# Kernel optimization log

Measured on AMD Instinct MI355X. Metric: run time of the kernel, lower is better.

## Reference

```python
import jax, jax.numpy as jnp
import numpy as np

N_FRAMES = 64
N_ATOMS = 512
SEG_LEN = 1


def get_segments(n_atoms: int, length: int) -> np.ndarray:
    """All ordered pairs of chain segments (i,i+L),(j,j+L) that share no atoms (j-i>L)."""
    starts = np.arange(n_atoms - length)
    i, j = np.meshgrid(starts, starts, indexing='ij')
    mask = (j - i) > length
    i, j = i[mask], j[mask]
    return np.stack([i, i + length, j, j + length], axis=1).astype(np.int32)


def setup_inputs() -> dict:
    key = jax.random.key(0)
    xyz = jax.random.normal(key, (N_FRAMES, N_ATOMS, 3), dtype=jnp.float32)
    segments = jnp.asarray(get_segments(N_ATOMS, SEG_LEN))  # (P, 4) int32
    return {"xyz": xyz, "segments": segments}


def _unit(v):
    return v / jnp.linalg.norm(v, axis=-1, keepdims=True)


def reference(xyz, segments):
    # xyz: (F, N, 3); segments: (P, 4) = [i, i+L, j, j+L]
    p1 = xyz[:, segments[:, 0]]  # (F, P, 3)
    p2 = xyz[:, segments[:, 1]]
    p3 = xyz[:, segments[:, 2]]
    p4 = xyz[:, segments[:, 3]]

    r12 = p2 - p1
    r13 = p3 - p1
    r14 = p4 - p1
    r23 = p3 - p2
    r24 = p4 - p2
    r34 = p4 - p3

    # unit normals of the four faces of the tetrahedron spanned by the segment pair
    n1 = _unit(jnp.cross(r13, r14))
    n2 = _unit(jnp.cross(r14, r24))
    n3 = _unit(jnp.cross(r24, r23))
    n4 = _unit(jnp.cross(r23, r13))

    def asin_dot(a, b):
        return jnp.arcsin(jnp.clip(jnp.sum(a * b, axis=-1), -1.0, 1.0))

    # Gauss linking integral (Klenin & Langowski) per segment pair
    theta = asin_dot(n1, n2) + asin_dot(n2, n3) + asin_dot(n3, n4) + asin_dot(n4, n1)
    sign = jnp.sign(jnp.sum(jnp.cross(r34, r12) * r13, axis=-1))
    wr = theta * sign / (2.0 * jnp.pi)  # (F, P)
    return wr
```

## Files before the change

### kernel.cpp

```cpp
#include <hip/hip_runtime.h>
#include <math.h>

#define NFRAMES 64
#define NATOMS  512
#define NSEG    129795
#define NROWS   509
#define BLOCK   128
#define LDS_SLOTS 576

typedef float v2 __attribute__((ext_vector_type(2)));

__device__ __forceinline__ v2 v2s(float x) { v2 r; r.x = x; r.y = x; return r; }
__device__ __forceinline__ v2 vfma(v2 a, v2 b, v2 c) { return __builtin_elementwise_fma(a, b, c); }
__device__ __forceinline__ v2 vabs(v2 x) { v2 r; r.x = fabsf(x.x); r.y = fabsf(x.y); return r; }
__device__ __forceinline__ v2 vmin1(v2 a) { v2 r; r.x = fminf(a.x, 1.0f); r.y = fminf(a.y, 1.0f); return r; }
__device__ __forceinline__ v2 vsqrt_raw(v2 x) {
    v2 r; r.x = __builtin_amdgcn_sqrtf(x.x); r.y = __builtin_amdgcn_sqrtf(x.y); return r;
}
__device__ __forceinline__ v2 vrsq_raw(v2 x) {
    v2 r; r.x = __builtin_amdgcn_rsqf(x.x); r.y = __builtin_amdgcn_rsqf(x.y); return r;
}
__device__ __forceinline__ v2 vcopysign(v2 m, v2 s) {
    v2 r; r.x = copysignf(m.x, s.x); r.y = copysignf(m.y, s.y); return r;
}

__device__ __forceinline__ v2 vasin(v2 x) {
    v2 ax = vmin1(vabs(x));
    v2 p  = vfma(ax, vfma(ax, vfma(ax, v2s(-0.0187293f), v2s(0.0742610f)), v2s(-0.2121144f)), v2s(1.5707288f));
    v2 r  = v2s(1.57079632679f) - vsqrt_raw(v2s(1.0f) - ax) * p;
    return vcopysign(r, x);
}

struct v23 { v2 x, y, z; };

__device__ __forceinline__ v23 vsub(v23 a, v23 b) { return v23{a.x - b.x, a.y - b.y, a.z - b.z}; }
__device__ __forceinline__ v23 vcross(v23 a, v23 b) {
    return v23{ vfma(a.y, b.z, -(a.z * b.y)),
                vfma(a.z, b.x, -(a.x * b.z)),
                vfma(a.x, b.y, -(a.y * b.x)) };
}
__device__ __forceinline__ v2 vdot(v23 a, v23 b) {
    return vfma(a.x, b.x, vfma(a.y, b.y, a.z * b.z));
}

__device__ __forceinline__ v2 writhe2(const v23& p1, const v23& p2, const v23& p3, const v23& p4) {
    v23 r12 = vsub(p2, p1);
    v23 r13 = vsub(p3, p1);
    v23 r14 = vsub(p4, p1);
    v23 r23 = vsub(p3, p2);
    v23 r24 = vsub(p4, p2);
    v23 r34 = vsub(p4, p3);

    v23 c1 = vcross(r13, r14);
    v23 c2 = vcross(r14, r24);
    v23 c3 = vcross(r24, r23);
    v23 c4 = vcross(r23, r13);

    v2 in1 = vrsq_raw(vdot(c1, c1));
    v2 in2 = vrsq_raw(vdot(c2, c2));
    v2 in3 = vrsq_raw(vdot(c3, c3));
    v2 in4 = vrsq_raw(vdot(c4, c4));

    v2 d12 = vdot(c1, c2) * (in1 * in2);
    v2 d23 = vdot(c2, c3) * (in2 * in3);
    v2 d34 = vdot(c3, c4) * (in3 * in4);
    v2 d41 = vdot(c4, c1) * (in4 * in1);

    v2 theta = (vasin(d12) + vasin(d23)) + (vasin(d34) + vasin(d41));

    v2 sv = vdot(vcross(r34, r12), r13);
    v2 sgn;
    sgn.x = (sv.x > 0.0f) ? 1.0f : ((sv.x < 0.0f) ? -1.0f : 0.0f);
    sgn.y = (sv.y > 0.0f) ? 1.0f : ((sv.y < 0.0f) ? -1.0f : 0.0f);
    return theta * sgn * v2s(0.15915494309189535f);
}

__device__ __forceinline__ int slot_of(int a) { return a + (a >> 3); }

__global__ __launch_bounds__(BLOCK) void writhe_kernel(
    const float* __restrict__ xyz,
    float*       __restrict__ out)
{
    __shared__ float4 sp[LDS_SLOTS];

    const int i = blockIdx.x;
    const int f = blockIdx.y;
    const float* fx = xyz + (size_t)f * (NATOMS * 3);
    for (int a = threadIdx.x; a < NATOMS; a += BLOCK) {
        const float* g = fx + 3 * a;
        sp[slot_of(a)] = make_float4(g[0], g[1], g[2], 0.0f);
    }
    __syncthreads();

    const int len = NROWS - i;
    const int t4  = threadIdx.x * 4;
    if (t4 >= len) return;
    const int jb  = i + 2 + t4;

    float4 A0 = sp[slot_of(min(jb,     511))];
    float4 A1 = sp[slot_of(min(jb + 1, 511))];
    float4 A2 = sp[slot_of(min(jb + 2, 511))];
    float4 A3 = sp[slot_of(min(jb + 3, 511))];
    float4 A4 = sp[slot_of(min(jb + 4, 511))];

    float4 P1 = sp[slot_of(i)];
    float4 P2 = sp[slot_of(i + 1)];
    v23 p1{v2s(P1.x), v2s(P1.y), v2s(P1.z)};
    v23 p2{v2s(P2.x), v2s(P2.y), v2s(P2.z)};

    v23 p3A{{A0.x, A1.x}, {A0.y, A1.y}, {A0.z, A1.z}};
    v23 p4A{{A1.x, A2.x}, {A1.y, A2.y}, {A1.z, A2.z}};
    v23 p3B{{A2.x, A3.x}, {A2.y, A3.y}, {A2.z, A3.z}};
    v23 p4B{{A3.x, A4.x}, {A3.y, A4.y}, {A3.z, A4.z}};

    v2 wA = writhe2(p1, p2, p3A, p4A);
    v2 wB = writhe2(p1, p2, p3B, p4B);

    const int off  = NROWS * i - (i * (i - 1)) / 2;
    const size_t obase = (size_t)f * NSEG + off + t4;
    const int rem = len - t4;
    out[obase] = wA.x;
    if (rem > 1) out[obase + 1] = wA.y;
    if (rem > 2) out[obase + 2] = wB.x;
    if (rem > 3) out[obase + 3] = wB.y;
}

extern "C" void kernel_launch(void* const* d_in, const int* in_sizes, int n_in,
                              void* d_out, int out_size, void* d_ws, size_t ws_size,
                              hipStream_t stream) {
    const float* xyz = (const float*)d_in[0];
    float*       out = (float*)d_out;

    dim3 grid(NROWS, NFRAMES);
    writhe_kernel<<<grid, BLOCK, 0, stream>>>(xyz, out);
}
```

Baseline: 99.86 us.

## Pair short and long triangle rows per block to balance work

```diff
diff --git a/kernel.cpp b/kernel.cpp
--- a/kernel.cpp
+++ b/kernel.cpp
@@ -5,7 +5,8 @@
 #define NATOMS  512
 #define NSEG    129795
 #define NROWS   509
-#define BLOCK   128
+#define NBLK    255
+#define BLOCK   256
 #define LDS_SLOTS 576
 
 typedef float v2 __attribute__((ext_vector_type(2)));
@@ -83,7 +84,7 @@
 {
     __shared__ float4 sp[LDS_SLOTS];
 
-    const int i = blockIdx.x;
+    const int b = blockIdx.x;
     const int f = blockIdx.y;
     const float* fx = xyz + (size_t)f * (NATOMS * 3);
     for (int a = threadIdx.x; a < NATOMS; a += BLOCK) {
@@ -92,37 +93,37 @@
     }
     __syncthreads();
 
-    const int len = NROWS - i;
-    const int t4  = threadIdx.x * 4;
-    if (t4 >= len) return;
-    const int jb  = i + 2 + t4;
+    const int rowA = b;
+    const int rowB = 508 - b;
+    const int lenA = NROWS - rowA;
+    const int lenB = (rowB == rowA) ? 0 : NROWS - rowB;
+    const int na   = (lenA + 1) >> 1;
 
-    float4 A0 = sp[slot_of(min(jb,     511))];
-    float4 A1 = sp[slot_of(min(jb + 1, 511))];
-    float4 A2 = sp[slot_of(min(jb + 2, 511))];
-    float4 A3 = sp[slot_of(min(jb + 3, 511))];
-    float4 A4 = sp[slot_of(min(jb + 4, 511))];
+    const int t   = threadIdx.x;
+    const bool inA = (t < na);
+    const int row = inA ? rowA : rowB;
+    const int len = inA ? lenA : lenB;
+    const int k0  = (inA ? t : (t - na)) << 1;
+    if (k0 >= len) return;
 
-    float4 P1 = sp[slot_of(i)];
-    float4 P2 = sp[slot_of(i + 1)];
+    const int j0 = row + 2 + k0;
+    float4 A0 = sp[slot_of(j0)];
+    float4 A1 = sp[slot_of(j0 + 1)];
+    float4 A2 = sp[slot_of(min(j0 + 2, 511))];
+    float4 P1 = sp[slot_of(row)];
+    float4 P2 = sp[slot_of(row + 1)];
+
     v23 p1{v2s(P1.x), v2s(P1.y), v2s(P1.z)};
     v23 p2{v2s(P2.x), v2s(P2.y), v2s(P2.z)};
+    v23 p3{{A0.x, A1.x}, {A0.y, A1.y}, {A0.z, A1.z}};
+    v23 p4{{A1.x, A2.x}, {A1.y, A2.y}, {A1.z, A2.z}};
 
-    v23 p3A{{A0.x, A1.x}, {A0.y, A1.y}, {A0.z, A1.z}};
-    v23 p4A{{A1.x, A2.x}, {A1.y, A2.y}, {A1.z, A2.z}};
-    v23 p3B{{A2.x, A3.x}, {A2.y, A3.y}, {A2.z, A3.z}};
-    v23 p4B{{A3.x, A4.x}, {A3.y, A4.y}, {A3.z, A4.z}};
+    v2 w = writhe2(p1, p2, p3, p4);
 
-    v2 wA = writhe2(p1, p2, p3A, p4A);
-    v2 wB = writhe2(p1, p2, p3B, p4B);
-
-    const int off  = NROWS * i - (i * (i - 1)) / 2;
-    const size_t obase = (size_t)f * NSEG + off + t4;
-    const int rem = len - t4;
-    out[obase] = wA.x;
-    if (rem > 1) out[obase + 1] = wA.y;
-    if (rem > 2) out[obase + 2] = wB.x;
-    if (rem > 3) out[obase + 3] = wB.y;
+    const int off = NROWS * row - (row * (row - 1)) / 2;
+    const size_t base = (size_t)f * NSEG + off + k0;
+    out[base] = w.x;
+    if (k0 + 1 < len) out[base + 1] = w.y;
 }
 
 extern "C" void kernel_launch(void* const* d_in, const int* in_sizes, int n_in,
@@ -131,6 +132,6 @@
     const float* xyz = (const float*)d_in[0];
     float*       out = (float*)d_out;
 
-    dim3 grid(NROWS, NFRAMES);
+    dim3 grid(NBLK, NFRAMES);
     writhe_kernel<<<grid, BLOCK, 0, stream>>>(xyz, out);
 }
```

Result: faster. 87.94 us (-11.9%).
